# Optimization experiments

Measured on AMD Instinct MI355X. Metric: run time of the kernel, lower is better.

The kernel has to match this reference:

```python
import jax, jax.numpy as jnp
import numpy as np

LECUN_A = 1.7159
LECUN_B = 0.666


def lecun_tanh(x):
    return LECUN_A * jnp.tanh(LECUN_B * x)


def setup_inputs() -> dict:
    key = jax.random.key(0)
    ks = jax.random.split(key, 12)
    B, T, I, H, U = 128, 1024, 256, 512, 1024
    s_in = 1.0 / np.sqrt(I + H)
    s_u = 1.0 / np.sqrt(U)
    return {
        "input": jax.random.normal(ks[0], (B, T, I), jnp.float32),
        "hx": jax.random.normal(ks[1], (B, T, H), jnp.float32),
        "ts": jax.random.uniform(ks[2], (B, T), jnp.float32),
        "W0": jax.random.normal(ks[3], (I + H, U), jnp.float32) * s_in,
        "b0": jnp.zeros((U,), jnp.float32),
        "W1": jax.random.normal(ks[4], (U, U), jnp.float32) * s_u,
        "b1": jnp.zeros((U,), jnp.float32),
        "W_ff1": jax.random.normal(ks[5], (U, H), jnp.float32) * s_u,
        "b_ff1": jnp.zeros((H,), jnp.float32),
        "W_ff2": jax.random.normal(ks[6], (U, H), jnp.float32) * s_u,
        "b_ff2": jnp.zeros((H,), jnp.float32),
        "W_ta": jax.random.normal(ks[7], (U, H), jnp.float32) * s_u,
        "b_ta": jnp.zeros((H,), jnp.float32),
        "W_tb": jax.random.normal(ks[8], (U, H), jnp.float32) * s_u,
        "b_tb": jnp.zeros((H,), jnp.float32),
    }


def reference(input, hx, ts, W0, b0, W1, b1, W_ff1, b_ff1, W_ff2, b_ff2,
              W_ta, b_ta, W_tb, b_tb):
    # x: [B, T, I+H]
    x = jnp.concatenate([input, hx], axis=2)
    # backbone: Linear -> LeCun -> Linear -> LeCun
    x = lecun_tanh(jnp.einsum("btc,cu->btu", x, W0) + b0)
    x = lecun_tanh(jnp.einsum("btu,uv->btv", x, W1) + b1)
    # four parallel heads sharing x: [B, T, H] each
    ff1 = jnp.tanh(jnp.einsum("btu,uh->bth", x, W_ff1) + b_ff1)
    ff2 = jnp.tanh(jnp.einsum("btu,uh->bth", x, W_ff2) + b_ff2)
    t_a = jnp.einsum("btu,uh->bth", x, W_ta) + b_ta
    t_b = jnp.einsum("btu,uh->bth", x, W_tb) + b_tb
    # time-gated interpolation
    t_interp = jax.nn.sigmoid(t_a * ts[:, :, None] + t_b)
    new_hidden = ff1 * (1.0 - t_interp) + t_interp * ff2
    return new_hidden
```

## Files before the change

kernel.cpp:

```cpp
#include <hip/hip_runtime.h>
#include <hip/hip_bf16.h>


typedef unsigned short u16;
typedef __bf16 bf16x8_t __attribute__((ext_vector_type(8)));
typedef float f32x4_t __attribute__((ext_vector_type(4)));
typedef u16 u16x8_t __attribute__((ext_vector_type(8)));

#define M_TOTAL 131072

__device__ __forceinline__ u16 f2bf(float f) {
  union { float f; unsigned u; } v; v.f = f;
  unsigned r = v.u + 0x7FFFu + ((v.u >> 16) & 1u);
  return (u16)(r >> 16);
}

__device__ __forceinline__ float fast_tanh(float x) {
  x = fminf(15.f, fmaxf(-15.f, x));
  float e = __expf(2.f * x);
  return (e - 1.f) * __builtin_amdgcn_rcpf(e + 1.f);
}

__device__ __forceinline__ float fast_sigmoid(float x) {
  return __builtin_amdgcn_rcpf(1.f + __expf(-x));
}

__device__ __forceinline__ void gload_lds16(const void* g, void* l) {
  __builtin_amdgcn_global_load_lds(
      (const __attribute__((address_space(1))) unsigned int*)g,
      (__attribute__((address_space(3))) unsigned int*)l,
      16, 0, 0);
}


__global__ void prep_x(const float* __restrict__ inp, const float* __restrict__ hx,
                       u16* __restrict__ X) {
  const int total = M_TOTAL * 96;
  int stride = gridDim.x * blockDim.x;
  for (int v = blockIdx.x * blockDim.x + threadIdx.x; v < total; v += stride) {
    int m = v / 96; int c = v - m * 96;
    const float* src = (c < 32) ? (inp + (size_t)m * 256 + (c << 3))
                                : (hx + (size_t)m * 512 + ((size_t)(c - 32) << 3));
    f32x4_t a = *(const f32x4_t*)src;
    f32x4_t b = *(const f32x4_t*)(src + 4);
    u16x8_t o;
    o[0]=f2bf(a[0]); o[1]=f2bf(a[1]); o[2]=f2bf(a[2]); o[3]=f2bf(a[3]);
    o[4]=f2bf(b[0]); o[5]=f2bf(b[1]); o[6]=f2bf(b[2]); o[7]=f2bf(b[3]);
    *(u16x8_t*)(X + (size_t)m * 768 + (c << 3)) = o;
  }
}

__global__ void prep_w(const float* __restrict__ W0, const float* __restrict__ W1,
                       const float* __restrict__ Wf1, const float* __restrict__ Wf2,
                       const float* __restrict__ Wta, const float* __restrict__ Wtb,
                       const float* __restrict__ bf1, const float* __restrict__ bf2,
                       const float* __restrict__ bta, const float* __restrict__ btb,
                       u16* __restrict__ W0T, u16* __restrict__ W1T,
                       u16* __restrict__ WhT, float* __restrict__ biasi) {
  int id = blockIdx.x * blockDim.x + threadIdx.x;
  u16x8_t o;
  if (id < 98304) {
    int n = id / 96, k0 = (id - n * 96) << 3;
#pragma unroll
    for (int i = 0; i < 8; ++i) o[i] = f2bf(W0[(size_t)(k0 + i) * 1024 + n]);
    *(u16x8_t*)(W0T + (size_t)n * 768 + k0) = o;
  } else if (id < 229376) {
    int id2 = id - 98304; int n = id2 >> 7, k0 = (id2 & 127) << 3;
#pragma unroll
    for (int i = 0; i < 8; ++i) o[i] = f2bf(W1[(size_t)(k0 + i) * 1024 + n]);
    *(u16x8_t*)(W1T + (size_t)n * 1024 + k0) = o;
  } else if (id < 491520) {
    int id3 = id - 229376; int head = id3 >> 16; int id4 = id3 & 65535;
    int n = id4 >> 7, k0 = (id4 & 127) << 3;
    const float* W = (head == 0) ? Wf1 : (head == 1) ? Wf2 : (head == 2) ? Wta : Wtb;
#pragma unroll
    for (int i = 0; i < 8; ++i) o[i] = f2bf(W[(size_t)(k0 + i) * 512 + n]);
    int row = ((n >> 4) << 6) + head * 16 + (n & 15);
    *(u16x8_t*)(WhT + (size_t)row * 1024 + k0) = o;
  } else if (id < 492032) {
    int h = id - 491520;
    int base = ((h >> 4) << 6) + (h & 15);
    biasi[base +  0] = bf1[h];
    biasi[base + 16] = bf2[h];
    biasi[base + 32] = bta[h];
    biasi[base + 48] = btb[h];
  }
}


#define BARX()  do { __builtin_amdgcn_s_barrier(); __builtin_amdgcn_sched_barrier(0); } while(0)
#define LGKM0() do { asm volatile("s_waitcnt lgkmcnt(0)" ::: "memory"); __builtin_amdgcn_sched_barrier(0); } while(0)
#define WAITVM(n) do { asm volatile("s_waitcnt vmcnt(" #n ")" ::: "memory"); __builtin_amdgcn_sched_barrier(0); } while(0)

template<int K, int NI, int EPI>
__global__ __launch_bounds__(512, 2)
void gemm256(const u16* __restrict__ A, const u16* __restrict__ BT,
             const float* __restrict__ bias, const float* __restrict__ ts,
             void* __restrict__ Cout)
{
  constexpr int NTn = NI / 256;
  constexpr int NT = K / 32;
  constexpr int NWG = (M_TOTAL / 256) * NTn;
  __shared__ __align__(16) char smem[131072];

  const int bid0 = blockIdx.x;
  const int bid = (bid0 & 7) * (NWG >> 3) + (bid0 >> 3);
  const int mt = bid / NTn, nt = bid % NTn;
  const int tileM = mt * 256, tileN = nt * 256;

  const int tid = threadIdx.x;
  const int w = tid >> 6, l = tid & 63;
  const int wm = w >> 2, wn = w & 3;

  const int cbS = ((l & 3) << 4) ^ (((l >> 5) & 1) << 5);
  const int laneK = cbS >> 1;
  const int rA = 32 * w + (l >> 2);
  const u16* aS0 = A + (size_t)(tileM + rA) * K + laneK;
  const u16* aS1 = aS0 + (size_t)16 * K;
  const u16* bS0 = BT + (size_t)(tileN + rA) * K + laneK;
  const u16* bS1 = bS0 + (size_t)16 * K;
  char* ldsA = smem + (w << 11);
  char* ldsB = smem + 65536 + (w << 11);

  const int colRs = ((l >> 4) << 4) ^ (((l >> 3) & 1) << 5);
  const char* aRd = smem + (wm * 128 + (l & 15)) * 64 + colRs;
  const char* bRd = smem + 65536 + (wn * 64 + (l & 15)) * 64 + colRs;

  f32x4_t acc[8][4];
#pragma unroll
  for (int i = 0; i < 8; ++i)
#pragma unroll
    for (int j = 0; j < 4; ++j) acc[i][j] = f32x4_t{0.f, 0.f, 0.f, 0.f};

  bf16x8_t af[8], bfr[4];

#define STAGE_S(t) do { \
    const int sl_ = ((t) & 3) << 14; \
    gload_lds16(aS0 + (size_t)(t) * 32, ldsA + sl_); \
    gload_lds16(aS1 + (size_t)(t) * 32, ldsA + sl_ + 1024); \
    gload_lds16(bS0 + (size_t)(t) * 32, ldsB + sl_); \
    gload_lds16(bS1 + (size_t)(t) * 32, ldsB + sl_ + 1024); } while(0)

#define READ_S(s) do { \
    _Pragma("unroll") for (int n_ = 0; n_ < 4; ++n_) \
      bfr[n_] = *(const bf16x8_t*)(bRd + (s) * 16384 + n_ * 1024); \
    _Pragma("unroll") for (int m_ = 0; m_ < 8; ++m_) \
      af[m_] = *(const bf16x8_t*)(aRd + (s) * 16384 + m_ * 1024); } while(0)

#define MFMA32() do { \
    __builtin_amdgcn_s_setprio(1); \
    _Pragma("unroll") for (int m_ = 0; m_ < 8; ++m_) \
      _Pragma("unroll") for (int n_ = 0; n_ < 4; ++n_) \
        acc[m_][n_] = __builtin_amdgcn_mfma_f32_16x16x32_bf16( \
            af[m_], bfr[n_], acc[m_][n_], 0, 0, 0); \
    __builtin_amdgcn_s_setprio(0); } while(0)

#define STEP(s, vmn, DOST, t) do { \
    WAITVM(vmn); BARX(); \
    if (DOST) STAGE_S(t); \
    READ_S(s); \
    LGKM0(); \
    MFMA32(); } while(0)

  STAGE_S(0); STAGE_S(1); STAGE_S(2);

#pragma unroll 1
  for (int i = 0; i < NT - 4; i += 4) {
    STEP(0, 8, true, i + 3);
    STEP(1, 8, true, i + 4);
    STEP(2, 8, true, i + 5);
    STEP(3, 8, true, i + 6);
  }
  STEP(0, 8, true, NT - 1);
  STEP(1, 8, false, 0);
  STEP(2, 4, false, 0);
  STEP(3, 0, false, 0);

  const int colBase = tileN + wn * 64 + (l & 15);
  float bv[4];
  bv[0] = bias[colBase];      bv[1] = bias[colBase + 16];
  bv[2] = bias[colBase + 32]; bv[3] = bias[colBase + 48];

  if constexpr (EPI == 0) {
    u16* C = (u16*)Cout;
    const int rowB = tileM + wm * 128 + ((l >> 4) << 2);
#pragma unroll
    for (int m = 0; m < 8; ++m)
#pragma unroll
      for (int nn = 0; nn < 4; ++nn)
#pragma unroll
        for (int j = 0; j < 4; ++j) {
          float v = acc[m][nn][j] + bv[nn];
          float t = 1.7159f * fast_tanh(0.666f * v);
          C[(size_t)(rowB + m * 16 + j) * NI + colBase + nn * 16] = f2bf(t);
        }
  } else {
    const int hg = ((tileN + wn * 64) >> 6) * 16 + (l & 15);
    float* out = (float*)Cout;
#pragma unroll
    for (int m = 0; m < 8; ++m)
#pragma unroll
      for (int j = 0; j < 4; ++j) {
        const int rl = wm * 128 + m * 16 + ((l >> 4) << 2) + j;
        const float tsv = ts[tileM + rl];
        float ff1 = fast_tanh(acc[m][0][j] + bv[0]);
        float ff2 = fast_tanh(acc[m][1][j] + bv[1]);
        float s = fast_sigmoid((acc[m][2][j] + bv[2]) * tsv + (acc[m][3][j] + bv[3]));
        out[(size_t)(tileM + rl) * 512 + hg] = ff1 + s * (ff2 - ff1);
      }
  }
#undef STAGE_S
#undef READ_S
#undef MFMA32
#undef STEP
}


extern "C" void kernel_launch(void* const* d_in, const int* in_sizes, int n_in,
                              void* d_out, int out_size, void* d_ws, size_t ws_size,
                              hipStream_t stream) {
  const float* input = (const float*)d_in[0];
  const float* hx    = (const float*)d_in[1];
  const float* ts    = (const float*)d_in[2];
  const float* W0    = (const float*)d_in[3];
  const float* b0    = (const float*)d_in[4];
  const float* W1    = (const float*)d_in[5];
  const float* b1    = (const float*)d_in[6];
  const float* Wff1  = (const float*)d_in[7];
  const float* bff1  = (const float*)d_in[8];
  const float* Wff2  = (const float*)d_in[9];
  const float* bff2  = (const float*)d_in[10];
  const float* Wta   = (const float*)d_in[11];
  const float* bta   = (const float*)d_in[12];
  const float* Wtb   = (const float*)d_in[13];
  const float* btb   = (const float*)d_in[14];

  const size_t WS_NEEDED = 544743424ull;
  if (ws_size < WS_NEEDED) return;
  char* ws = (char*)d_ws;
  u16* Xcat = (u16*)(ws);
  u16* X2   = (u16*)(ws);
  u16* X1   = (u16*)(ws + 268435456ull);
  u16* W0T  = (u16*)(ws + 536870912ull);
  u16* W1T  = (u16*)(ws + 538443776ull);
  u16* WhT  = (u16*)(ws + 540540928ull);
  float* biasi = (float*)(ws + 544735232ull);

  prep_x<<<2048, 256, 0, stream>>>(input, hx, Xcat);
  prep_w<<<1922, 256, 0, stream>>>(W0, W1, Wff1, Wff2, Wta, Wtb,
                                   bff1, bff2, bta, btb, W0T, W1T, WhT, biasi);

  gemm256<768, 1024, 0><<<2048, 512, 0, stream>>>(Xcat, W0T, b0, nullptr, X1);
  gemm256<1024, 1024, 0><<<2048, 512, 0, stream>>>(X1, W1T, b1, nullptr, X2);
  gemm256<1024, 2048, 1><<<4096, 512, 0, stream>>>(X2, WhT, biasi, ts, d_out);
}
```

Baseline: 1.243 ms.

## Pre-pack weights in MFMA fragment order and load B directly into registers

Weights are now pre-packed in MFMA fragment order, so each lane can load its B fragments straight from global memory into registers and only the A operand is staged through LDS. Tiles shrink to 128x256, which cuts LDS use from 128KB to 32KB and lets launch bounds allow 4 blocks per CU with twice as many workgroups. B registers are double-buffered, with loads issued after the MFMAs of each step. The trade-off is more global or L2 traffic for B, since it is no longer shared through LDS across the M-waves, and less M reuse per tile.

```diff
diff --git a/kernel.cpp b/kernel.cpp
--- a/kernel.cpp
+++ b/kernel.cpp
@@ -55,28 +55,35 @@
                        const float* __restrict__ Wta, const float* __restrict__ Wtb,
                        const float* __restrict__ bf1, const float* __restrict__ bf2,
                        const float* __restrict__ bta, const float* __restrict__ btb,
-                       u16* __restrict__ W0T, u16* __restrict__ W1T,
-                       u16* __restrict__ WhT, float* __restrict__ biasi) {
+                       u16* __restrict__ W0P, u16* __restrict__ W1P,
+                       u16* __restrict__ WhP, float* __restrict__ biasi) {
   int id = blockIdx.x * blockDim.x + threadIdx.x;
   u16x8_t o;
   if (id < 98304) {
-    int n = id / 96, k0 = (id - n * 96) << 3;
-#pragma unroll
-    for (int i = 0; i < 8; ++i) o[i] = f2bf(W0[(size_t)(k0 + i) * 1024 + n]);
-    *(u16x8_t*)(W0T + (size_t)n * 768 + k0) = o;
+    int l = id & 63, r = id >> 6;
+    int g = r % 64, t = r / 64;
+    int col = g * 16 + (l & 15), kb = t * 32 + ((l >> 4) << 3);
+#pragma unroll
+    for (int e = 0; e < 8; ++e) o[e] = f2bf(W0[(size_t)(kb + e) * 1024 + col]);
+    *((u16x8_t*)W0P + id) = o;
   } else if (id < 229376) {
-    int id2 = id - 98304; int n = id2 >> 7, k0 = (id2 & 127) << 3;
-#pragma unroll
-    for (int i = 0; i < 8; ++i) o[i] = f2bf(W1[(size_t)(k0 + i) * 1024 + n]);
-    *(u16x8_t*)(W1T + (size_t)n * 1024 + k0) = o;
+    int id2 = id - 98304;
+    int l = id2 & 63, r = id2 >> 6;
+    int g = r & 63, t = r >> 6;
+    int col = g * 16 + (l & 15), kb = t * 32 + ((l >> 4) << 3);
+#pragma unroll
+    for (int e = 0; e < 8; ++e) o[e] = f2bf(W1[(size_t)(kb + e) * 1024 + col]);
+    *((u16x8_t*)W1P + id2) = o;
   } else if (id < 491520) {
-    int id3 = id - 229376; int head = id3 >> 16; int id4 = id3 & 65535;
-    int n = id4 >> 7, k0 = (id4 & 127) << 3;
+    int id3 = id - 229376;
+    int l = id3 & 63, r = id3 >> 6;
+    int g = r & 127, t = r >> 7;
+    int head = g & 3;
+    int n = (g >> 2) * 16 + (l & 15), kb = t * 32 + ((l >> 4) << 3);
     const float* W = (head == 0) ? Wf1 : (head == 1) ? Wf2 : (head == 2) ? Wta : Wtb;
 #pragma unroll
-    for (int i = 0; i < 8; ++i) o[i] = f2bf(W[(size_t)(k0 + i) * 512 + n]);
-    int row = ((n >> 4) << 6) + head * 16 + (n & 15);
-    *(u16x8_t*)(WhT + (size_t)row * 1024 + k0) = o;
+    for (int e = 0; e < 8; ++e) o[e] = f2bf(W[(size_t)(kb + e) * 512 + n]);
+    *((u16x8_t*)WhP + id3) = o;
   } else if (id < 492032) {
     int h = id - 491520;
     int base = ((h >> 4) << 6) + (h & 15);
@@ -88,93 +95,105 @@
 }
 
 
-#define BARX()  do { __builtin_amdgcn_s_barrier(); __builtin_amdgcn_sched_barrier(0); } while(0)
-#define LGKM0() do { asm volatile("s_waitcnt lgkmcnt(0)" ::: "memory"); __builtin_amdgcn_sched_barrier(0); } while(0)
-#define WAITVM(n) do { asm volatile("s_waitcnt vmcnt(" #n ")" ::: "memory"); __builtin_amdgcn_sched_barrier(0); } while(0)
+#define BARX()   do { __builtin_amdgcn_s_barrier(); __builtin_amdgcn_sched_barrier(0); } while(0)
+#define LGKM0()  do { asm volatile("s_waitcnt lgkmcnt(0)" ::: "memory"); __builtin_amdgcn_sched_barrier(0); } while(0)
+#define SCHEDB() __builtin_amdgcn_sched_barrier(0)
+#define WAITVM_(n) do { asm volatile("s_waitcnt vmcnt(" #n ")" ::: "memory"); __builtin_amdgcn_sched_barrier(0); } while(0)
+#define WAITVM(n) WAITVM_(n)
 
 template<int K, int NI, int EPI>
-__global__ __launch_bounds__(512, 2)
-void gemm256(const u16* __restrict__ A, const u16* __restrict__ BT,
-             const float* __restrict__ bias, const float* __restrict__ ts,
-             void* __restrict__ Cout)
+__global__ __launch_bounds__(512, 4)
+void gemmB(const u16* __restrict__ A, const char* __restrict__ Bp,
+           const float* __restrict__ bias, const float* __restrict__ ts,
+           void* __restrict__ Cout)
 {
   constexpr int NTn = NI / 256;
+  constexpr int G64 = NI / 16;
+  constexpr size_t G64K = (size_t)G64 * 1024;
   constexpr int NT = K / 32;
-  constexpr int NWG = (M_TOTAL / 256) * NTn;
-  __shared__ __align__(16) char smem[131072];
-
-  const int bid0 = blockIdx.x;
-  const int bid = (bid0 & 7) * (NWG >> 3) + (bid0 >> 3);
+  constexpr int NWG = (M_TOTAL / 128) * NTn;
+  __shared__ __align__(16) char smem[32768];
+
+  const int bid = ((blockIdx.x & 7) * (NWG >> 3)) + (blockIdx.x >> 3);
   const int mt = bid / NTn, nt = bid % NTn;
-  const int tileM = mt * 256, tileN = nt * 256;
-
-  const int tid = threadIdx.x;
-  const int w = tid >> 6, l = tid & 63;
+  const int tileM = mt * 128, tileN = nt * 256;
+
+  const int tid = threadIdx.x, w = tid >> 6, l = tid & 63;
   const int wm = w >> 2, wn = w & 3;
 
-  const int cbS = ((l & 3) << 4) ^ (((l >> 5) & 1) << 5);
-  const int laneK = cbS >> 1;
-  const int rA = 32 * w + (l >> 2);
-  const u16* aS0 = A + (size_t)(tileM + rA) * K + laneK;
-  const u16* aS1 = aS0 + (size_t)16 * K;
-  const u16* bS0 = BT + (size_t)(tileN + rA) * K + laneK;
-  const u16* bS1 = bS0 + (size_t)16 * K;
-  char* ldsA = smem + (w << 11);
-  char* ldsB = smem + 65536 + (w << 11);
-
+  const int laneK = ((l & 3) << 3) ^ (((l >> 5) & 1) << 4);
+  const u16* aS = A + (size_t)(tileM + 16 * w + (l >> 2)) * K + laneK;
+  char* ldsW = smem + (w << 10);
   const int colRs = ((l >> 4) << 4) ^ (((l >> 3) & 1) << 5);
-  const char* aRd = smem + (wm * 128 + (l & 15)) * 64 + colRs;
-  const char* bRd = smem + 65536 + (wn * 64 + (l & 15)) * 64 + colRs;
-
-  f32x4_t acc[8][4];
-#pragma unroll
-  for (int i = 0; i < 8; ++i)
+  const char* aRd = smem + (wm * 64 + (l & 15)) * 64 + colRs;
+  const char* bp0 = Bp + ((size_t)(((tileN >> 4) + wn * 4) * 64 + l) << 4);
+
+  f32x4_t acc[4][4];
+#pragma unroll
+  for (int i = 0; i < 4; ++i)
 #pragma unroll
     for (int j = 0; j < 4; ++j) acc[i][j] = f32x4_t{0.f, 0.f, 0.f, 0.f};
 
-  bf16x8_t af[8], bfr[4];
-
-#define STAGE_S(t) do { \
-    const int sl_ = ((t) & 3) << 14; \
-    gload_lds16(aS0 + (size_t)(t) * 32, ldsA + sl_); \
-    gload_lds16(aS1 + (size_t)(t) * 32, ldsA + sl_ + 1024); \
-    gload_lds16(bS0 + (size_t)(t) * 32, ldsB + sl_); \
-    gload_lds16(bS1 + (size_t)(t) * 32, ldsB + sl_ + 1024); } while(0)
-
-#define READ_S(s) do { \
-    _Pragma("unroll") for (int n_ = 0; n_ < 4; ++n_) \
-      bfr[n_] = *(const bf16x8_t*)(bRd + (s) * 16384 + n_ * 1024); \
-    _Pragma("unroll") for (int m_ = 0; m_ < 8; ++m_) \
-      af[m_] = *(const bf16x8_t*)(aRd + (s) * 16384 + m_ * 1024); } while(0)
-
-#define MFMA32() do { \
+  bf16x8_t af[4], ba[4], bb[4];
+
+#define GSTEP(W1N, SLOT, BK, DOST, STPTR, STSLOT, DOBL, BLPTR) do { \
+    WAITVM(W1N); BARX(); \
+    if (DOST) gload_lds16((STPTR), ldsW + (STSLOT) * 8192); \
+    af[0] = *(const bf16x8_t*)(aRd + (SLOT) * 8192 +    0); \
+    af[1] = *(const bf16x8_t*)(aRd + (SLOT) * 8192 + 1024); \
+    af[2] = *(const bf16x8_t*)(aRd + (SLOT) * 8192 + 2048); \
+    af[3] = *(const bf16x8_t*)(aRd + (SLOT) * 8192 + 3072); \
+    LGKM0(); \
     __builtin_amdgcn_s_setprio(1); \
-    _Pragma("unroll") for (int m_ = 0; m_ < 8; ++m_) \
+    _Pragma("unroll") for (int m_ = 0; m_ < 4; ++m_) \
       _Pragma("unroll") for (int n_ = 0; n_ < 4; ++n_) \
         acc[m_][n_] = __builtin_amdgcn_mfma_f32_16x16x32_bf16( \
-            af[m_], bfr[n_], acc[m_][n_], 0, 0, 0); \
-    __builtin_amdgcn_s_setprio(0); } while(0)
-
-#define STEP(s, vmn, DOST, t) do { \
-    WAITVM(vmn); BARX(); \
-    if (DOST) STAGE_S(t); \
-    READ_S(s); \
-    LGKM0(); \
-    MFMA32(); } while(0)
-
-  STAGE_S(0); STAGE_S(1); STAGE_S(2);
-
+            af[m_], BK[n_], acc[m_][n_], 0, 0, 0); \
+    __builtin_amdgcn_s_setprio(0); \
+    SCHEDB(); \
+    if (DOBL) { \
+      BK[0] = *(const bf16x8_t*)((BLPTR)); \
+      BK[1] = *(const bf16x8_t*)((BLPTR) + 1024); \
+      BK[2] = *(const bf16x8_t*)((BLPTR) + 2048); \
+      BK[3] = *(const bf16x8_t*)((BLPTR) + 3072); \
+    } \
+    SCHEDB(); \
+  } while(0)
+
+  ba[0] = *(const bf16x8_t*)(bp0);
+  ba[1] = *(const bf16x8_t*)(bp0 + 1024);
+  ba[2] = *(const bf16x8_t*)(bp0 + 2048);
+  ba[3] = *(const bf16x8_t*)(bp0 + 3072);
+  bb[0] = *(const bf16x8_t*)(bp0 + G64K);
+  bb[1] = *(const bf16x8_t*)(bp0 + G64K + 1024);
+  bb[2] = *(const bf16x8_t*)(bp0 + G64K + 2048);
+  bb[3] = *(const bf16x8_t*)(bp0 + G64K + 3072);
+  SCHEDB();
+  gload_lds16(aS,      ldsW);
+  gload_lds16(aS + 32, ldsW + 8192);
+  gload_lds16(aS + 64, ldsW + 16384);
+  SCHEDB();
+
+  GSTEP(2,  0, ba, 1, aS +  96, 3, 1, bp0 + 2 * G64K);
+  GSTEP(6,  1, bb, 1, aS + 128, 0, 1, bp0 + 3 * G64K);
+  GSTEP(10, 2, ba, 1, aS + 160, 1, 1, bp0 + 4 * G64K);
+  GSTEP(14, 3, bb, 1, aS + 192, 2, 1, bp0 + 5 * G64K);
+
+  const u16* aSt = aS + 7 * 32;
+  const char* bSt = bp0 + 6 * G64K;
 #pragma unroll 1
-  for (int i = 0; i < NT - 4; i += 4) {
-    STEP(0, 8, true, i + 3);
-    STEP(1, 8, true, i + 4);
-    STEP(2, 8, true, i + 5);
-    STEP(3, 8, true, i + 6);
-  }
-  STEP(0, 8, true, NT - 1);
-  STEP(1, 8, false, 0);
-  STEP(2, 4, false, 0);
-  STEP(3, 0, false, 0);
+  for (int it = 0; it < (NT - 8) / 4; ++it) {
+    GSTEP(14, 0, ba, 1, aSt,      3, 1, bSt);
+    GSTEP(14, 1, bb, 1, aSt + 32, 0, 1, bSt + G64K);
+    GSTEP(14, 2, ba, 1, aSt + 64, 1, 1, bSt + 2 * G64K);
+    GSTEP(14, 3, bb, 1, aSt + 96, 2, 1, bSt + 3 * G64K);
+    aSt += 128; bSt += 4 * G64K;
+  }
+
+  GSTEP(14, 0, ba, 1, aS + (size_t)(NT - 1) * 32, 3, 1, bp0 + (size_t)(NT - 2) * G64K);
+  GSTEP(14, 1, bb, 0, aS, 0, 1, bp0 + (size_t)(NT - 1) * G64K);
+  GSTEP(13, 2, ba, 0, aS, 0, 0, bp0);
+  GSTEP(8,  3, bb, 0, aS, 0, 0, bp0);
 
   const int colBase = tileN + wn * 64 + (l & 15);
   float bv[4];
@@ -183,9 +202,9 @@
 
   if constexpr (EPI == 0) {
     u16* C = (u16*)Cout;
-    const int rowB = tileM + wm * 128 + ((l >> 4) << 2);
-#pragma unroll
-    for (int m = 0; m < 8; ++m)
+    const int rowB = tileM + wm * 64 + ((l >> 4) << 2);
+#pragma unroll
+    for (int m = 0; m < 4; ++m)
 #pragma unroll
       for (int nn = 0; nn < 4; ++nn)
 #pragma unroll
@@ -198,10 +217,10 @@
     const int hg = ((tileN + wn * 64) >> 6) * 16 + (l & 15);
     float* out = (float*)Cout;
 #pragma unroll
-    for (int m = 0; m < 8; ++m)
+    for (int m = 0; m < 4; ++m)
 #pragma unroll
       for (int j = 0; j < 4; ++j) {
-        const int rl = wm * 128 + m * 16 + ((l >> 4) << 2) + j;
+        const int rl = wm * 64 + m * 16 + ((l >> 4) << 2) + j;
         const float tsv = ts[tileM + rl];
         float ff1 = fast_tanh(acc[m][0][j] + bv[0]);
         float ff2 = fast_tanh(acc[m][1][j] + bv[1]);
@@ -209,10 +228,7 @@
         out[(size_t)(tileM + rl) * 512 + hg] = ff1 + s * (ff2 - ff1);
       }
   }
-#undef STAGE_S
-#undef READ_S
-#undef MFMA32
-#undef STEP
+#undef GSTEP
 }
 
 
@@ -241,16 +257,16 @@
   u16* Xcat = (u16*)(ws);
   u16* X2   = (u16*)(ws);
   u16* X1   = (u16*)(ws + 268435456ull);
-  u16* W0T  = (u16*)(ws + 536870912ull);
-  u16* W1T  = (u16*)(ws + 538443776ull);
-  u16* WhT  = (u16*)(ws + 540540928ull);
+  u16* W0P  = (u16*)(ws + 536870912ull);
+  u16* W1P  = (u16*)(ws + 538443776ull);
+  u16* WhP  = (u16*)(ws + 540540928ull);
   float* biasi = (float*)(ws + 544735232ull);
 
   prep_x<<<2048, 256, 0, stream>>>(input, hx, Xcat);
   prep_w<<<1922, 256, 0, stream>>>(W0, W1, Wff1, Wff2, Wta, Wtb,
-                                   bff1, bff2, bta, btb, W0T, W1T, WhT, biasi);
-
-  gemm256<768, 1024, 0><<<2048, 512, 0, stream>>>(Xcat, W0T, b0, nullptr, X1);
-  gemm256<1024, 1024, 0><<<2048, 512, 0, stream>>>(X1, W1T, b1, nullptr, X2);
-  gemm256<1024, 2048, 1><<<4096, 512, 0, stream>>>(X2, WhT, biasi, ts, d_out);
-}
+                                   bff1, bff2, bta, btb, W0P, W1P, WhP, biasi);
+
+  gemmB<768, 1024, 0><<<4096, 512, 0, stream>>>(Xcat, (const char*)W0P, b0, nullptr, X1);
+  gemmB<1024, 1024, 0><<<4096, 512, 0, stream>>>(X1, (const char*)W1P, b1, nullptr, X2);
+  gemmB<1024, 2048, 1><<<8192, 512, 0, stream>>>(X2, (const char*)WhP, biasi, ts, d_out);
+}
```

After: 1.608 ms. +29.3%, slower.

## Shrink GEMM tile to 256x128 with 4 waves and 3-stage LDS pipeline

Applied to the files above, without the earlier changes.

Replaces the 256x256, 8-wave GEMM with a 256x128, 4-wave workgroup. Each wave still computes a 128x64 output block. The four-slot LDS ring becomes a three-slot ring of 24 KB each, cutting shared memory from 128 KB to 72 KB, and twice as many workgroups are launched. The goal is more resident workgroups and better latency hiding. The cost is lower reuse of the A tile, since A is now reloaded for every 128-column tile, and a shallower prefetch depth.

```diff
diff --git a/kernel.cpp b/kernel.cpp
--- a/kernel.cpp
+++ b/kernel.cpp
@@ -88,43 +88,40 @@
 }
 
 
-#define BARX()  do { __builtin_amdgcn_s_barrier(); __builtin_amdgcn_sched_barrier(0); } while(0)
-#define LGKM0() do { asm volatile("s_waitcnt lgkmcnt(0)" ::: "memory"); __builtin_amdgcn_sched_barrier(0); } while(0)
-#define WAITVM(n) do { asm volatile("s_waitcnt vmcnt(" #n ")" ::: "memory"); __builtin_amdgcn_sched_barrier(0); } while(0)
+#define BARX()   do { __builtin_amdgcn_s_barrier(); __builtin_amdgcn_sched_barrier(0); } while(0)
+#define LGKM0()  do { asm volatile("s_waitcnt lgkmcnt(0)" ::: "memory"); __builtin_amdgcn_sched_barrier(0); } while(0)
+#define SCHEDB() __builtin_amdgcn_sched_barrier(0)
+#define WAITVM_(n) do { asm volatile("s_waitcnt vmcnt(" #n ")" ::: "memory"); __builtin_amdgcn_sched_barrier(0); } while(0)
+#define WAITVM(n) WAITVM_(n)
 
 template<int K, int NI, int EPI>
-__global__ __launch_bounds__(512, 2)
-void gemm256(const u16* __restrict__ A, const u16* __restrict__ BT,
-             const float* __restrict__ bias, const float* __restrict__ ts,
-             void* __restrict__ Cout)
+__global__ __launch_bounds__(256, 2)
+void gemmR(const u16* __restrict__ A, const u16* __restrict__ BT,
+           const float* __restrict__ bias, const float* __restrict__ ts,
+           void* __restrict__ Cout)
 {
-  constexpr int NTn = NI / 256;
+  constexpr int NTn = NI / 128;
   constexpr int NT = K / 32;
   constexpr int NWG = (M_TOTAL / 256) * NTn;
-  __shared__ __align__(16) char smem[131072];
-
-  const int bid0 = blockIdx.x;
-  const int bid = (bid0 & 7) * (NWG >> 3) + (bid0 >> 3);
+  constexpr int JMAIN = (NT == 24) ? 21 : 30;
+  __shared__ __align__(16) char smem[73728];
+
+  const int bid = ((blockIdx.x & 7) * (NWG >> 3)) + (blockIdx.x >> 3);
   const int mt = bid / NTn, nt = bid % NTn;
-  const int tileM = mt * 256, tileN = nt * 256;
-
-  const int tid = threadIdx.x;
-  const int w = tid >> 6, l = tid & 63;
-  const int wm = w >> 2, wn = w & 3;
-
-  const int cbS = ((l & 3) << 4) ^ (((l >> 5) & 1) << 5);
-  const int laneK = cbS >> 1;
-  const int rA = 32 * w + (l >> 2);
-  const u16* aS0 = A + (size_t)(tileM + rA) * K + laneK;
-  const u16* aS1 = aS0 + (size_t)16 * K;
-  const u16* bS0 = BT + (size_t)(tileN + rA) * K + laneK;
-  const u16* bS1 = bS0 + (size_t)16 * K;
-  char* ldsA = smem + (w << 11);
-  char* ldsB = smem + 65536 + (w << 11);
+  const int tileM = mt * 256, tileN = nt * 128;
+
+  const int tid = threadIdx.x, w = tid >> 6, l = tid & 63;
+  const int wm = w >> 1, wn = w & 1;
+
+  const int laneK = ((l & 3) << 3) ^ (((l >> 5) & 1) << 4);
+  const u16* aS = A + (size_t)(tileM + 64 * w + (l >> 2)) * K + laneK;
+  const u16* bS = BT + (size_t)(tileN + 32 * w + (l >> 2)) * K + laneK;
+  char* ldsA = smem + (w << 12);
+  char* ldsB = smem + 16384 + (w << 11);
 
   const int colRs = ((l >> 4) << 4) ^ (((l >> 3) & 1) << 5);
   const char* aRd = smem + (wm * 128 + (l & 15)) * 64 + colRs;
-  const char* bRd = smem + 65536 + (wn * 64 + (l & 15)) * 64 + colRs;
+  const char* bRd = smem + 16384 + (wn * 64 + (l & 15)) * 64 + colRs;
 
   f32x4_t acc[8][4];
 #pragma unroll
@@ -133,48 +130,49 @@
     for (int j = 0; j < 4; ++j) acc[i][j] = f32x4_t{0.f, 0.f, 0.f, 0.f};
 
   bf16x8_t af[8], bfr[4];
-
-#define STAGE_S(t) do { \
-    const int sl_ = ((t) & 3) << 14; \
-    gload_lds16(aS0 + (size_t)(t) * 32, ldsA + sl_); \
-    gload_lds16(aS1 + (size_t)(t) * 32, ldsA + sl_ + 1024); \
-    gload_lds16(bS0 + (size_t)(t) * 32, ldsB + sl_); \
-    gload_lds16(bS1 + (size_t)(t) * 32, ldsB + sl_ + 1024); } while(0)
-
-#define READ_S(s) do { \
+  int kOff = 0;
+
+#define STAGE6(SLOT) do { \
+    gload_lds16(aS + kOff,          ldsA + (SLOT) * 24576); \
+    gload_lds16(aS + kOff + 16 * K, ldsA + (SLOT) * 24576 + 1024); \
+    gload_lds16(aS + kOff + 32 * K, ldsA + (SLOT) * 24576 + 2048); \
+    gload_lds16(aS + kOff + 48 * K, ldsA + (SLOT) * 24576 + 3072); \
+    gload_lds16(bS + kOff,          ldsB + (SLOT) * 24576); \
+    gload_lds16(bS + kOff + 16 * K, ldsB + (SLOT) * 24576 + 1024); \
+    kOff += 32; } while(0)
+
+#define STEP(SLOT, STSLOT, WVN, DOST) do { \
+    WAITVM(WVN); BARX(); \
+    if (DOST) STAGE6(STSLOT); \
+    _Pragma("unroll") for (int m_ = 0; m_ < 8; ++m_) \
+      af[m_] = *(const bf16x8_t*)(aRd + (SLOT) * 24576 + m_ * 1024); \
     _Pragma("unroll") for (int n_ = 0; n_ < 4; ++n_) \
-      bfr[n_] = *(const bf16x8_t*)(bRd + (s) * 16384 + n_ * 1024); \
-    _Pragma("unroll") for (int m_ = 0; m_ < 8; ++m_) \
-      af[m_] = *(const bf16x8_t*)(aRd + (s) * 16384 + m_ * 1024); } while(0)
-
-#define MFMA32() do { \
+      bfr[n_] = *(const bf16x8_t*)(bRd + (SLOT) * 24576 + n_ * 1024); \
+    LGKM0(); \
     __builtin_amdgcn_s_setprio(1); \
     _Pragma("unroll") for (int m_ = 0; m_ < 8; ++m_) \
       _Pragma("unroll") for (int n_ = 0; n_ < 4; ++n_) \
         acc[m_][n_] = __builtin_amdgcn_mfma_f32_16x16x32_bf16( \
             af[m_], bfr[n_], acc[m_][n_], 0, 0, 0); \
-    __builtin_amdgcn_s_setprio(0); } while(0)
-
-#define STEP(s, vmn, DOST, t) do { \
-    WAITVM(vmn); BARX(); \
-    if (DOST) STAGE_S(t); \
-    READ_S(s); \
-    LGKM0(); \
-    MFMA32(); } while(0)
-
-  STAGE_S(0); STAGE_S(1); STAGE_S(2);
+    __builtin_amdgcn_s_setprio(0); \
+  } while(0)
+
+  STAGE6(0); STAGE6(1);
 
 #pragma unroll 1
-  for (int i = 0; i < NT - 4; i += 4) {
-    STEP(0, 8, true, i + 3);
-    STEP(1, 8, true, i + 4);
-    STEP(2, 8, true, i + 5);
-    STEP(3, 8, true, i + 6);
-  }
-  STEP(0, 8, true, NT - 1);
-  STEP(1, 8, false, 0);
-  STEP(2, 4, false, 0);
-  STEP(3, 0, false, 0);
+  for (int it = 0; it < JMAIN / 3; ++it) {
+    STEP(0, 2, 6, true);
+    STEP(1, 0, 6, true);
+    STEP(2, 1, 6, true);
+  }
+  if constexpr (NT == 24) {
+    STEP(0, 2, 6, true);
+    STEP(1, 0, 6, false);
+    STEP(2, 0, 0, false);
+  } else {
+    STEP(0, 0, 6, false);
+    STEP(1, 0, 0, false);
+  }
 
   const int colBase = tileN + wn * 64 + (l & 15);
   float bv[4];
@@ -209,9 +207,7 @@
         out[(size_t)(tileM + rl) * 512 + hg] = ff1 + s * (ff2 - ff1);
       }
   }
-#undef STAGE_S
-#undef READ_S
-#undef MFMA32
+#undef STAGE6
 #undef STEP
 }
 
@@ -250,7 +246,7 @@
   prep_w<<<1922, 256, 0, stream>>>(W0, W1, Wff1, Wff2, Wta, Wtb,
                                    bff1, bff2, bta, btb, W0T, W1T, WhT, biasi);
 
-  gemm256<768, 1024, 0><<<2048, 512, 0, stream>>>(Xcat, W0T, b0, nullptr, X1);
-  gemm256<1024, 1024, 0><<<2048, 512, 0, stream>>>(X1, W1T, b1, nullptr, X2);
-  gemm256<1024, 2048, 1><<<4096, 512, 0, stream>>>(X2, WhT, biasi, ts, d_out);
-}
+  gemmR<768, 1024, 0><<<4096, 256, 0, stream>>>(Xcat, W0T, b0, nullptr, X1);
+  gemmR<1024, 1024, 0><<<4096, 256, 0, stream>>>(X1, W1T, b1, nullptr, X2);
+  gemmR<1024, 2048, 1><<<8192, 256, 0, stream>>>(X2, WhT, biasi, ts, d_out);
+}
```

Measured after the change: 1.300 ms. +4.6%, slower.
